# Optimization experiments

Hardware: AMD Instinct MI355X
Metric: run time of the kernel (lower is better)

## Reference

```python
import jax, jax.numpy as jnp
import numpy as np

NUM_BUCKETS = 32
MAX_DISTANCE = 128


def _rel_bucket(relative_position):
    """T5 relative-position bucketing, bidirectional=False (causal)."""
    n = jnp.maximum(-relative_position, 0)  # distance looking back
    max_exact = NUM_BUCKETS // 2
    is_small = n < max_exact
    nf = jnp.maximum(n.astype(jnp.float32), 1.0)
    val_large = max_exact + (
        jnp.log(nf / max_exact) / np.log(MAX_DISTANCE / max_exact)
        * (NUM_BUCKETS - max_exact)
    ).astype(jnp.int32)
    val_large = jnp.minimum(val_large, NUM_BUCKETS - 1)
    return jnp.where(is_small, n, val_large)


def setup_inputs() -> dict:
    key = jax.random.key(0)
    B, L, E, H, D, F = 4, 2048, 1024, 16, 64, 4096
    ks = jax.random.split(key, 8)
    inputs = jax.random.normal(ks[0], (B, L, E), jnp.float32)
    wq = jax.random.normal(ks[1], (E, H, D), jnp.float32) * (E ** -0.5)
    wk = jax.random.normal(ks[2], (E, H, D), jnp.float32) * (E ** -0.5)
    wv = jax.random.normal(ks[3], (E, H, D), jnp.float32) * (E ** -0.5)
    wo = jax.random.normal(ks[4], (H, D, E), jnp.float32) * ((H * D) ** -0.5)
    wi = jax.random.normal(ks[5], (E, F), jnp.float32) * (E ** -0.5)
    wmo = jax.random.normal(ks[6], (F, E), jnp.float32) * (F ** -0.5)
    rel_emb = jax.random.normal(ks[7], (NUM_BUCKETS, H), jnp.float32)
    decoder_mask = jnp.tril(jnp.ones((L, L), bool))[None, None]  # causal [1,1,L,L]
    return dict(inputs=inputs, wq=wq, wk=wk, wv=wv, wo=wo, wi=wi,
                wmo=wmo, rel_emb=rel_emb, decoder_mask=decoder_mask)


def reference(inputs, wq, wk, wv, wo, wi, wmo, rel_emb, decoder_mask):
    B, L, E = inputs.shape
    # --- T5 relative position bias: [1, H, L, L] ---
    pos = jnp.arange(L)
    rp = pos[None, :] - pos[:, None]  # memory_pos - query_pos
    bias = rel_emb[_rel_bucket(rp)]               # [L, L, H]
    bias = jnp.transpose(bias, (2, 0, 1))[None]   # [1, H, L, L]

    # NOTE: the provided source computes LayerNorm into `x` but feeds the raw
    # `inputs` (as lnx) to attention and MLP; we follow the source literally.
    lnx = inputs

    # --- self attention with additive relpos bias ---
    q = jnp.einsum('ble,ehd->blhd', lnx, wq)
    k = jnp.einsum('ble,ehd->blhd', lnx, wk)
    v = jnp.einsum('ble,ehd->blhd', lnx, wv)
    D = q.shape[-1]
    scores = jnp.einsum('bqhd,bkhd->bhqk', q, k) / jnp.sqrt(jnp.asarray(D, q.dtype))
    scores = scores + bias
    scores = jnp.where(decoder_mask, scores, jnp.finfo(scores.dtype).min)
    probs = jax.nn.softmax(scores, axis=-1)
    ctx = jnp.einsum('bhqk,bkhd->bqhd', probs, v)
    attn = jnp.einsum('bqhd,hde->bqe', ctx, wo)

    # --- parallel MLP (relu) off the same lnx ---
    mlp = jnp.einsum('blf,fe->ble', jax.nn.relu(jnp.einsum('ble,ef->blf', lnx, wi)), wmo)

    # residual sum (dropout deterministic -> no-op)
    return inputs + mlp + attn
```

## Files before the change

kernel.cpp:

```cpp
#include <hip/hip_runtime.h>
#include <stdint.h>

typedef short bf16x8 __attribute__((ext_vector_type(8)));
typedef float f32x4 __attribute__((ext_vector_type(4)));

__device__ __forceinline__ short f2bf(float f) {
  unsigned int u = __float_as_uint(f);
  u = (u + 0x7FFFu + ((u >> 16) & 1u)) >> 16;
  return (short)u;
}

__device__ __forceinline__ void gload_lds16(const void* g, void* l) {
  __builtin_amdgcn_global_load_lds((const __attribute__((address_space(1))) void*)g,
                                   (__attribute__((address_space(3))) void*)l, 16, 0, 0);
}
__device__ __forceinline__ void gload_lds4(const void* g, void* l) {
  __builtin_amdgcn_global_load_lds((const __attribute__((address_space(1))) void*)g,
                                   (__attribute__((address_space(3))) void*)l, 4, 0, 0);
}


__global__ void cvt_x_kernel(const float* __restrict__ in, short* __restrict__ out) {
  int i = blockIdx.x * 256 + threadIdx.x;
  float4 v = ((const float4*)in)[i];
  short4 o;
  o.x = f2bf(v.x); o.y = f2bf(v.y); o.z = f2bf(v.z); o.w = f2bf(v.w);
  ((short4*)out)[i] = o;
}

__global__ void transpose_f2b_kernel(const float* __restrict__ in, short* __restrict__ out,
                                     int R, int C, int ldout) {
  __shared__ float tile[32][33];
  int tx = threadIdx.x & 31, ty = threadIdx.x >> 5;
  int c0 = blockIdx.x * 32, r0 = blockIdx.y * 32;
#pragma unroll
  for (int j = 0; j < 4; j++)
    tile[ty + j * 8][tx] = in[(size_t)(r0 + ty + j * 8) * C + c0 + tx];
  __syncthreads();
#pragma unroll
  for (int j = 0; j < 4; j++)
    out[(size_t)(c0 + ty + j * 8) * ldout + r0 + tx] = f2bf(tile[tx][ty + j * 8]);
}

__global__ void transpose_v_kernel(const short* __restrict__ qkv, short* __restrict__ vT) {
  __shared__ short tile[32][33];
  int tx = threadIdx.x & 31, ty = threadIdx.x >> 5;
  int l0 = blockIdx.x * 32, d0 = blockIdx.y * 32;
  int bh = blockIdx.z, b = bh >> 4, h = bh & 15;
#pragma unroll
  for (int j = 0; j < 4; j++)
    tile[ty + j * 8][tx] =
        qkv[(size_t)(b * 2048 + l0 + ty + j * 8) * 3072 + 2048 + h * 64 + d0 + tx];
  __syncthreads();
#pragma unroll
  for (int j = 0; j < 4; j++)
    vT[((size_t)bh * 64 + d0 + ty + j * 8) * 2048 + l0 + tx] = tile[tx][ty + j * 8];
}

__global__ void bias_kernel(const float* __restrict__ rel_emb, float* __restrict__ btab) {
  int i = blockIdx.x * 256 + threadIdx.x;
  int h = i >> 11, n = i & 2047;
  int bucket;
  if (n < 16) {
    bucket = n;
  } else {
    float t = logf((float)n * 0.0625f) * (16.0f / 2.0794415416798357f);
    bucket = 16 + (int)t;
    if (bucket > 31) bucket = 31;
  }
  btab[i] = rel_emb[bucket * 16 + h] * 1.4426950408889634f - 28.853900817779268f;
}

template <int EPI>
__global__ __launch_bounds__(256, 3)
void gemm_bt_kernel(const short* __restrict__ A, const short* __restrict__ Bt,
                    int N, int K, short* __restrict__ Cb) {
  __shared__ short lA[128 * 64];
  __shared__ short lB[128 * 64];
  const int t = threadIdx.x;
  const int w = t >> 6, lane = t & 63;
  const int q4 = lane >> 4, l15 = lane & 15;
  const int mBase = blockIdx.y * 128, nBase = blockIdx.x * 128;
  const int wm = (w >> 1) * 64, wn = (w & 1) * 64;

  const f32x4 fzero = {0.f, 0.f, 0.f, 0.f};
  f32x4 acc[4][4];
#pragma unroll
  for (int i = 0; i < 4; i++)
#pragma unroll
    for (int j = 0; j < 4; j++) acc[i][j] = fzero;

  for (int k0 = 0; k0 < K; k0 += 64) {
    __syncthreads();
#pragma unroll
    for (int p = 0; p < 4; p++) {
      int c = p * 256 + t;
      int row = c >> 3;
      int kc = ((c & 7) - row) & 7;
      gload_lds16(A + (size_t)(mBase + row) * K + k0 + kc * 8, lA + (size_t)(c - lane) * 8);
      gload_lds16(Bt + (size_t)(nBase + row) * K + k0 + kc * 8, lB + (size_t)(c - lane) * 8);
    }
    __syncthreads();
#pragma unroll
    for (int ks = 0; ks < 2; ks++) {
      bf16x8 af[4], bfr[4];
#pragma unroll
      for (int mi = 0; mi < 4; mi++) {
        int row = wm + mi * 16 + l15;
        af[mi] = *(const bf16x8*)&lA[row * 64 + ((ks * 4 + q4 + row) & 7) * 8];
      }
#pragma unroll
      for (int ni = 0; ni < 4; ni++) {
        int row = wn + ni * 16 + l15;
        bfr[ni] = *(const bf16x8*)&lB[row * 64 + ((ks * 4 + q4 + row) & 7) * 8];
      }
#pragma unroll
      for (int mi = 0; mi < 4; mi++)
#pragma unroll
        for (int ni = 0; ni < 4; ni++)
          acc[mi][ni] =
              __builtin_amdgcn_mfma_f32_16x16x32_bf16(af[mi], bfr[ni], acc[mi][ni], 0, 0, 0);
    }
  }

#pragma unroll
  for (int mi = 0; mi < 4; mi++)
#pragma unroll
    for (int ni = 0; ni < 4; ni++) {
#pragma unroll
      for (int r = 0; r < 4; r++) {
        size_t idx = (size_t)(mBase + wm + mi * 16 + q4 * 4 + r) * N +
                     (nBase + wn + ni * 16 + l15);
        float v = acc[mi][ni][r];
        if constexpr (EPI == 0) Cb[idx] = f2bf(v);
        else Cb[idx] = f2bf(v > 0.f ? v : 0.f);
      }
    }
}

__global__ __launch_bounds__(256, 3)
void gemm_cat_kernel(const short* __restrict__ ctx, const short* __restrict__ hidden,
                     const short* __restrict__ wcat, const float* __restrict__ resid,
                     float* __restrict__ out) {
  __shared__ short lA[128 * 64];
  __shared__ short lB[128 * 64];
  const int t = threadIdx.x;
  const int w = t >> 6, lane = t & 63;
  const int q4 = lane >> 4, l15 = lane & 15;
  const int mBase = blockIdx.y * 128, nBase = blockIdx.x * 128;
  const int wm = (w >> 1) * 64, wn = (w & 1) * 64;

  const f32x4 fzero = {0.f, 0.f, 0.f, 0.f};
  f32x4 acc[4][4];
#pragma unroll
  for (int i = 0; i < 4; i++)
#pragma unroll
    for (int j = 0; j < 4; j++) acc[i][j] = fzero;

  for (int k0 = 0; k0 < 5120; k0 += 64) {
    const short* Abase = (k0 < 1024) ? (ctx + k0) : (hidden + (k0 - 1024));
    const size_t lda = (k0 < 1024) ? 1024 : 4096;
    __syncthreads();
#pragma unroll
    for (int p = 0; p < 4; p++) {
      int c = p * 256 + t;
      int row = c >> 3;
      int kc = ((c & 7) - row) & 7;
      gload_lds16(Abase + (size_t)(mBase + row) * lda + kc * 8, lA + (size_t)(c - lane) * 8);
      gload_lds16(wcat + (size_t)(nBase + row) * 5120 + k0 + kc * 8,
                  lB + (size_t)(c - lane) * 8);
    }
    __syncthreads();
#pragma unroll
    for (int ks = 0; ks < 2; ks++) {
      bf16x8 af[4], bfr[4];
#pragma unroll
      for (int mi = 0; mi < 4; mi++) {
        int row = wm + mi * 16 + l15;
        af[mi] = *(const bf16x8*)&lA[row * 64 + ((ks * 4 + q4 + row) & 7) * 8];
      }
#pragma unroll
      for (int ni = 0; ni < 4; ni++) {
        int row = wn + ni * 16 + l15;
        bfr[ni] = *(const bf16x8*)&lB[row * 64 + ((ks * 4 + q4 + row) & 7) * 8];
      }
#pragma unroll
      for (int mi = 0; mi < 4; mi++)
#pragma unroll
        for (int ni = 0; ni < 4; ni++)
          acc[mi][ni] =
              __builtin_amdgcn_mfma_f32_16x16x32_bf16(af[mi], bfr[ni], acc[mi][ni], 0, 0, 0);
    }
  }

#pragma unroll
  for (int mi = 0; mi < 4; mi++)
#pragma unroll
    for (int ni = 0; ni < 4; ni++) {
#pragma unroll
      for (int r = 0; r < 4; r++) {
        size_t idx = (size_t)(mBase + wm + mi * 16 + q4 * 4 + r) * 1024 +
                     (nBase + wn + ni * 16 + l15);
        out[idx] = acc[mi][ni][r] + resid[idx];
      }
    }
}

__global__ __launch_bounds__(256, 3)
void attn_kernel(const short* __restrict__ qkv, const short* __restrict__ vT,
                 const float* __restrict__ bias_tab, short* __restrict__ ctx) {
  __shared__ short lK[128 * 64];
  __shared__ short lV[64 * 128];
  __shared__ short lP[4][16 * 128];
  __shared__ float lBias[192];

  const int t = threadIdx.x, w = t >> 6, lane = t & 63;
  const int q4 = lane >> 4, l15 = lane & 15;
  const int bh = blockIdx.x;
  const int qt = 31 - blockIdx.y;
  const int b = bh >> 4, h = bh & 15;
  const int q0 = qt * 64;
  const int ntiles = (qt + 2) >> 1;
  const f32x4 fzero = {0.f, 0.f, 0.f, 0.f};
  const float C1 = 0.125f * 1.4426950408889634f;

  const size_t qrow = (size_t)(b * 2048 + q0 + w * 16 + l15) * 3072 + h * 64;
  bf16x8 aq0 = *(const bf16x8*)(qkv + qrow + q4 * 8);
  bf16x8 aq1 = *(const bf16x8*)(qkv + qrow + 32 + q4 * 8);

  f32x4 vacc[4];
#pragma unroll
  for (int db = 0; db < 4; db++) vacc[db] = fzero;
  float l_part[4] = {0.f, 0.f, 0.f, 0.f};

  const float* btab = bias_tab + h * 2048;
  const int qrow0 = q0 + w * 16 + q4 * 4;
  const int bofs = w * 16 + q4 * 4 + 127 - l15;

  for (int kt = 0; kt < ntiles; kt++) {
    __syncthreads();
#pragma unroll
    for (int p = 0; p < 4; p++) {
      int c = p * 256 + t;
      int row = c >> 3;
      int kc = ((c & 7) - row) & 7;
      gload_lds16(qkv + (size_t)(b * 2048 + kt * 128 + row) * 3072 + 1024 + h * 64 + kc * 8,
                  lK + (size_t)(c - lane) * 8);
    }
#pragma unroll
    for (int p = 0; p < 4; p++) {
      int c = p * 256 + t;
      int d = c >> 4;
      int vc = ((c & 15) - d) & 15;
      gload_lds16(vT + ((size_t)bh * 64 + d) * 2048 + kt * 128 + vc * 8,
                  lV + (size_t)(c - lane) * 8);
    }
    if (w < 3) {
      int d = q0 - kt * 128 - 127 + t;
      d = d < 0 ? 0 : (d > 2047 ? 2047 : d);
      gload_lds4(btab + d, lBias + (t - lane));
    }
    __syncthreads();

    float pr[8][4];
#pragma unroll
    for (int nb = 0; nb < 8; nb++) {
      int row = nb * 16 + l15;
      bf16x8 bk0 = *(const bf16x8*)&lK[row * 64 + ((q4 + row) & 7) * 8];
      bf16x8 bk1 = *(const bf16x8*)&lK[row * 64 + ((q4 + 4 + row) & 7) * 8];
      f32x4 f = fzero;
      f = __builtin_amdgcn_mfma_f32_16x16x32_bf16(aq0, bk0, f, 0, 0, 0);
      f = __builtin_amdgcn_mfma_f32_16x16x32_bf16(aq1, bk1, f, 0, 0, 0);
      const int kcol = kt * 128 + row;
#pragma unroll
      for (int r = 0; r < 4; r++) {
        int dist = (qrow0 + r) - kcol;
        float tv = f[r] * C1 + lBias[bofs + r - nb * 16];
        float pv = __builtin_amdgcn_exp2f(tv);
        pv = (dist < 0) ? 0.f : pv;
        pr[nb][r] = pv;
        l_part[r] += pv;
      }
    }

    short* lPw = lP[w];
#pragma unroll
    for (int nb = 0; nb < 8; nb++) {
      int c = nb * 2 + (l15 >> 3);
#pragma unroll
      for (int r = 0; r < 4; r++) {
        int row = q4 * 4 + r;
        lPw[row * 128 + ((c + row) & 15) * 8 + (l15 & 7)] = f2bf(pr[nb][r]);
      }
    }

    bf16x8 ap[4];
#pragma unroll
    for (int ks2 = 0; ks2 < 4; ks2++)
      ap[ks2] = *(const bf16x8*)&lPw[l15 * 128 + ((ks2 * 4 + q4 + l15) & 15) * 8];
#pragma unroll
    for (int db = 0; db < 4; db++) {
      int row = db * 16 + l15;
#pragma unroll
      for (int ks2 = 0; ks2 < 4; ks2++) {
        bf16x8 bv = *(const bf16x8*)&lV[row * 128 + ((ks2 * 4 + q4 + row) & 15) * 8];
        vacc[db] = __builtin_amdgcn_mfma_f32_16x16x32_bf16(ap[ks2], bv, vacc[db], 0, 0, 0);
      }
    }
  }

  float inv[4];
#pragma unroll
  for (int r = 0; r < 4; r++) {
    float ps = l_part[r];
    ps += __shfl_xor(ps, 1);
    ps += __shfl_xor(ps, 2);
    ps += __shfl_xor(ps, 4);
    ps += __shfl_xor(ps, 8);
    inv[r] = 1.0f / ps;
  }
#pragma unroll
  for (int db = 0; db < 4; db++)
#pragma unroll
    for (int r = 0; r < 4; r++) {
      size_t idx = (size_t)(b * 2048 + q0 + w * 16 + q4 * 4 + r) * 1024 +
                   h * 64 + db * 16 + l15;
      ctx[idx] = f2bf(vacc[db][r] * inv[r]);
    }
}

extern "C" void kernel_launch(void* const* d_in, const int* in_sizes, int n_in,
                              void* d_out, int out_size, void* d_ws, size_t ws_size,
                              hipStream_t stream) {
  (void)in_sizes; (void)n_in; (void)out_size; (void)ws_size;
  const float* inputs  = (const float*)d_in[0];
  const float* wq      = (const float*)d_in[1];
  const float* wk      = (const float*)d_in[2];
  const float* wv      = (const float*)d_in[3];
  const float* wo      = (const float*)d_in[4];
  const float* wi      = (const float*)d_in[5];
  const float* wmo     = (const float*)d_in[6];
  const float* rel_emb = (const float*)d_in[7];
  float* out = (float*)d_out;
  char* ws = (char*)d_ws;

  const size_t MB = 1ull << 20;
  short* x16    = (short*)(ws + 0);
  short* qkv    = (short*)(ws + 16 * MB);
  short* hidden = (short*)(ws + 16 * MB);
  short* vT     = (short*)(ws + 64 * MB);
  short* wqkvt  = (short*)(ws + 80 * MB);
  short* wit    = (short*)(ws + 86 * MB);
  short* wcat   = (short*)(ws + 94 * MB);
  float* btab   = (float*)(ws + 105 * MB);
  short* ctx    = (short*)(ws + 106 * MB);

  cvt_x_kernel<<<8192, 256, 0, stream>>>(inputs, x16);
  transpose_f2b_kernel<<<dim3(32, 32), 256, 0, stream>>>(wq, wqkvt, 1024, 1024, 1024);
  transpose_f2b_kernel<<<dim3(32, 32), 256, 0, stream>>>(wk, wqkvt + 1024 * 1024, 1024, 1024, 1024);
  transpose_f2b_kernel<<<dim3(32, 32), 256, 0, stream>>>(wv, wqkvt + 2 * 1024 * 1024, 1024, 1024, 1024);
  transpose_f2b_kernel<<<dim3(128, 32), 256, 0, stream>>>(wi, wit, 1024, 4096, 1024);
  transpose_f2b_kernel<<<dim3(32, 32), 256, 0, stream>>>(wo, wcat, 1024, 1024, 5120);
  transpose_f2b_kernel<<<dim3(32, 128), 256, 0, stream>>>(wmo, wcat + 1024, 4096, 1024, 5120);
  bias_kernel<<<128, 256, 0, stream>>>(rel_emb, btab);

  gemm_bt_kernel<0><<<dim3(24, 64), 256, 0, stream>>>(x16, wqkvt, 3072, 1024, qkv);
  transpose_v_kernel<<<dim3(64, 2, 64), 256, 0, stream>>>(qkv, vT);
  attn_kernel<<<dim3(64, 32), 256, 0, stream>>>(qkv, vT, btab, ctx);
  gemm_bt_kernel<1><<<dim3(32, 64), 256, 0, stream>>>(x16, wit, 4096, 1024, hidden);
  gemm_cat_kernel<<<dim3(8, 64), 256, 0, stream>>>(ctx, hidden, wcat, inputs, out);
}
```

Before: 489.8 us.

## Merge prep kernels into one launch and fuse QKV with MLP-up GEMM

All weight transposes, the input conversion and the bias-table build now run in a single prep kernel that dispatches on block index, replacing eight launches. When the workspace is large enough, the QKV projection and the MLP up-projection run as one GEMM over a concatenated weight, with the epilogue routing columns to qkv or hidden and applying ReLU for the MLP part. This is meant to cut launch overhead and fill the GPU better with a larger grid. The workspace is re-laid out so that ctx aliases x16, and a fallback path keeps the old split when the workspace is small.

```diff
diff --git a/kernel.cpp b/kernel.cpp
--- a/kernel.cpp
+++ b/kernel.cpp
@@ -19,20 +19,51 @@
                                    (__attribute__((address_space(3))) void*)l, 4, 0, 0);
 }
 
-
-__global__ void cvt_x_kernel(const float* __restrict__ in, short* __restrict__ out) {
-  int i = blockIdx.x * 256 + threadIdx.x;
-  float4 v = ((const float4*)in)[i];
-  short4 o;
-  o.x = f2bf(v.x); o.y = f2bf(v.y); o.z = f2bf(v.z); o.w = f2bf(v.w);
-  ((short4*)out)[i] = o;
-}
-
-__global__ void transpose_f2b_kernel(const float* __restrict__ in, short* __restrict__ out,
-                                     int R, int C, int ldout) {
+__global__ void prep_kernel(const float* __restrict__ inputs, const float* __restrict__ wq,
+                            const float* __restrict__ wk, const float* __restrict__ wv,
+                            const float* __restrict__ wi, const float* __restrict__ wo,
+                            const float* __restrict__ wmo, const float* __restrict__ rel_emb,
+                            short* __restrict__ x16, short* __restrict__ wcat1,
+                            short* __restrict__ wcat, float* __restrict__ btab) {
+  const int t = threadIdx.x;
+  int id = blockIdx.x;
+
+  if (id < 8192) {
+    int i = id * 256 + t;
+    float4 v = ((const float4*)inputs)[i];
+    short4 o;
+    o.x = f2bf(v.x); o.y = f2bf(v.y); o.z = f2bf(v.z); o.w = f2bf(v.w);
+    ((short4*)x16)[i] = o;
+    return;
+  }
+  id -= 8192;
+
+  if (id >= 12288) {
+    int i = (id - 12288) * 256 + t;
+    int h = i >> 11, n = i & 2047;
+    int bucket;
+    if (n < 16) {
+      bucket = n;
+    } else {
+      float tv = logf((float)n * 0.0625f) * (16.0f / 2.0794415416798357f);
+      bucket = 16 + (int)tv;
+      if (bucket > 31) bucket = 31;
+    }
+    btab[i] = rel_emb[bucket * 16 + h] * 1.4426950408889634f - 28.853900817779268f;
+    return;
+  }
+
+  const float* in; short* out; int C, ldout, bx, by;
+  if (id < 1024)      { in = wq;  out = wcat1;                C = 1024; ldout = 1024; int r = id;         bx = r & 31;  by = r >> 5; }
+  else if (id < 2048) { in = wk;  out = wcat1 + 1024 * 1024;  C = 1024; ldout = 1024; int r = id - 1024;  bx = r & 31;  by = r >> 5; }
+  else if (id < 3072) { in = wv;  out = wcat1 + 2048 * 1024;  C = 1024; ldout = 1024; int r = id - 2048;  bx = r & 31;  by = r >> 5; }
+  else if (id < 7168) { in = wi;  out = wcat1 + 3072 * 1024;  C = 4096; ldout = 1024; int r = id - 3072;  bx = r & 127; by = r >> 7; }
+  else if (id < 8192) { in = wo;  out = wcat;                 C = 1024; ldout = 5120; int r = id - 7168;  bx = r & 31;  by = r >> 5; }
+  else                { in = wmo; out = wcat + 1024;          C = 1024; ldout = 5120; int r = id - 8192;  bx = r & 31;  by = r >> 5; }
+
   __shared__ float tile[32][33];
-  int tx = threadIdx.x & 31, ty = threadIdx.x >> 5;
-  int c0 = blockIdx.x * 32, r0 = blockIdx.y * 32;
+  int tx = t & 31, ty = t >> 5;
+  int c0 = bx * 32, r0 = by * 32;
 #pragma unroll
   for (int j = 0; j < 4; j++)
     tile[ty + j * 8][tx] = in[(size_t)(r0 + ty + j * 8) * C + c0 + tx];
@@ -57,31 +88,17 @@
     vT[((size_t)bh * 64 + d0 + ty + j * 8) * 2048 + l0 + tx] = tile[tx][ty + j * 8];
 }
 
-__global__ void bias_kernel(const float* __restrict__ rel_emb, float* __restrict__ btab) {
-  int i = blockIdx.x * 256 + threadIdx.x;
-  int h = i >> 11, n = i & 2047;
-  int bucket;
-  if (n < 16) {
-    bucket = n;
-  } else {
-    float t = logf((float)n * 0.0625f) * (16.0f / 2.0794415416798357f);
-    bucket = 16 + (int)t;
-    if (bucket > 31) bucket = 31;
-  }
-  btab[i] = rel_emb[bucket * 16 + h] * 1.4426950408889634f - 28.853900817779268f;
-}
-
-template <int EPI>
 __global__ __launch_bounds__(256, 3)
-void gemm_bt_kernel(const short* __restrict__ A, const short* __restrict__ Bt,
-                    int N, int K, short* __restrict__ Cb) {
+void gemm_qkvmlp_kernel(const short* __restrict__ A, const short* __restrict__ Bt,
+                        short* __restrict__ qkv, short* __restrict__ hidden, int xoff) {
   __shared__ short lA[128 * 64];
   __shared__ short lB[128 * 64];
   const int t = threadIdx.x;
   const int w = t >> 6, lane = t & 63;
   const int q4 = lane >> 4, l15 = lane & 15;
-  const int mBase = blockIdx.y * 128, nBase = blockIdx.x * 128;
+  const int mBase = blockIdx.y * 128, nBase = (blockIdx.x + xoff) * 128;
   const int wm = (w >> 1) * 64, wn = (w & 1) * 64;
+  const int K = 1024;
 
   const f32x4 fzero = {0.f, 0.f, 0.f, 0.f};
   f32x4 acc[4][4];
@@ -123,17 +140,21 @@
     }
   }
 
+  const bool isMlp = nBase >= 3072;
+  short* Cb = isMlp ? hidden : qkv;
+  const int ldC = isMlp ? 4096 : 3072;
+  const int ncol = isMlp ? nBase - 3072 : nBase;
 #pragma unroll
   for (int mi = 0; mi < 4; mi++)
 #pragma unroll
     for (int ni = 0; ni < 4; ni++) {
 #pragma unroll
       for (int r = 0; r < 4; r++) {
-        size_t idx = (size_t)(mBase + wm + mi * 16 + q4 * 4 + r) * N +
-                     (nBase + wn + ni * 16 + l15);
+        size_t idx = (size_t)(mBase + wm + mi * 16 + q4 * 4 + r) * ldC +
+                     (ncol + wn + ni * 16 + l15);
         float v = acc[mi][ni][r];
-        if constexpr (EPI == 0) Cb[idx] = f2bf(v);
-        else Cb[idx] = f2bf(v > 0.f ? v : 0.f);
+        if (isMlp && v < 0.f) v = 0.f;
+        Cb[idx] = f2bf(v);
       }
     }
 }
@@ -332,7 +353,7 @@
 extern "C" void kernel_launch(void* const* d_in, const int* in_sizes, int n_in,
                               void* d_out, int out_size, void* d_ws, size_t ws_size,
                               hipStream_t stream) {
-  (void)in_sizes; (void)n_in; (void)out_size; (void)ws_size;
+  (void)in_sizes; (void)n_in; (void)out_size;
   const float* inputs  = (const float*)d_in[0];
   const float* wq      = (const float*)d_in[1];
   const float* wk      = (const float*)d_in[2];
@@ -343,30 +364,42 @@
   const float* rel_emb = (const float*)d_in[7];
   float* out = (float*)d_out;
   char* ws = (char*)d_ws;
-
   const size_t MB = 1ull << 20;
-  short* x16    = (short*)(ws + 0);
-  short* qkv    = (short*)(ws + 16 * MB);
-  short* hidden = (short*)(ws + 16 * MB);
-  short* vT     = (short*)(ws + 64 * MB);
-  short* wqkvt  = (short*)(ws + 80 * MB);
-  short* wit    = (short*)(ws + 86 * MB);
-  short* wcat   = (short*)(ws + 94 * MB);
-  float* btab   = (float*)(ws + 105 * MB);
-  short* ctx    = (short*)(ws + 106 * MB);
-
-  cvt_x_kernel<<<8192, 256, 0, stream>>>(inputs, x16);
-  transpose_f2b_kernel<<<dim3(32, 32), 256, 0, stream>>>(wq, wqkvt, 1024, 1024, 1024);
-  transpose_f2b_kernel<<<dim3(32, 32), 256, 0, stream>>>(wk, wqkvt + 1024 * 1024, 1024, 1024, 1024);
-  transpose_f2b_kernel<<<dim3(32, 32), 256, 0, stream>>>(wv, wqkvt + 2 * 1024 * 1024, 1024, 1024, 1024);
-  transpose_f2b_kernel<<<dim3(128, 32), 256, 0, stream>>>(wi, wit, 1024, 4096, 1024);
-  transpose_f2b_kernel<<<dim3(32, 32), 256, 0, stream>>>(wo, wcat, 1024, 1024, 5120);
-  transpose_f2b_kernel<<<dim3(32, 128), 256, 0, stream>>>(wmo, wcat + 1024, 4096, 1024, 5120);
-  bias_kernel<<<128, 256, 0, stream>>>(rel_emb, btab);
-
-  gemm_bt_kernel<0><<<dim3(24, 64), 256, 0, stream>>>(x16, wqkvt, 3072, 1024, qkv);
-  transpose_v_kernel<<<dim3(64, 2, 64), 256, 0, stream>>>(qkv, vT);
-  attn_kernel<<<dim3(64, 32), 256, 0, stream>>>(qkv, vT, btab, ctx);
-  gemm_bt_kernel<1><<<dim3(32, 64), 256, 0, stream>>>(x16, wit, 4096, 1024, hidden);
+  const bool big = ws_size >= 171 * MB;
+
+  short *x16, *qkv, *hidden, *vT, *wcat1, *wcat, *ctx;
+  float* btab;
+  if (big) {
+    x16    = (short*)(ws + 0);
+    ctx    = (short*)(ws + 0);
+    qkv    = (short*)(ws + 16 * MB);
+    vT     = (short*)(ws + 64 * MB);
+    hidden = (short*)(ws + 80 * MB);
+    wcat1  = (short*)(ws + 144 * MB);
+    wcat   = (short*)(ws + 158 * MB);
+    btab   = (float*)(ws + 169 * MB);
+  } else {
+    x16    = (short*)(ws + 0);
+    qkv    = (short*)(ws + 16 * MB);
+    hidden = (short*)(ws + 16 * MB);
+    vT     = (short*)(ws + 64 * MB);
+    wcat1  = (short*)(ws + 80 * MB);
+    wcat   = (short*)(ws + 94 * MB);
+    btab   = (float*)(ws + 105 * MB);
+    ctx    = (short*)(ws + 106 * MB);
+  }
+
+  prep_kernel<<<20608, 256, 0, stream>>>(inputs, wq, wk, wv, wi, wo, wmo, rel_emb,
+                                         x16, wcat1, wcat, btab);
+  if (big) {
+    gemm_qkvmlp_kernel<<<dim3(56, 64), 256, 0, stream>>>(x16, wcat1, qkv, hidden, 0);
+    transpose_v_kernel<<<dim3(64, 2, 64), 256, 0, stream>>>(qkv, vT);
+    attn_kernel<<<dim3(64, 32), 256, 0, stream>>>(qkv, vT, btab, ctx);
+  } else {
+    gemm_qkvmlp_kernel<<<dim3(24, 64), 256, 0, stream>>>(x16, wcat1, qkv, hidden, 0);
+    transpose_v_kernel<<<dim3(64, 2, 64), 256, 0, stream>>>(qkv, vT);
+    attn_kernel<<<dim3(64, 32), 256, 0, stream>>>(qkv, vT, btab, ctx);
+    gemm_qkvmlp_kernel<<<dim3(32, 64), 256, 0, stream>>>(x16, wcat1, qkv, hidden, 24);
+  }
   gemm_cat_kernel<<<dim3(8, 64), 256, 0, stream>>>(ctx, hidden, wcat, inputs, out);
 }
```

Result: faster. 441.7 us (-9.8%).
